# Performance work log

Hardware: AMD Instinct MI355X
Metric: run time of the kernel (lower is better)

Reference implementation:

```python
import jax, jax.numpy as jnp
import numpy as np

DIM, NH, T_MAX = 1024, 16, 2048
HD = DIM // NH
EPS = 1e-6


def _rope_tables(T, hd, dtype=jnp.float32):
    inv_freq = 1.0 / (10000.0 ** (jnp.arange(0, hd, 2, dtype=jnp.float32) / hd))
    t = jnp.arange(T, dtype=jnp.float32)
    freqs = jnp.outer(t, inv_freq)                 # [T, hd/2]
    emb = jnp.concatenate([freqs, freqs], axis=-1)  # [T, hd]
    return jnp.cos(emb).astype(dtype), jnp.sin(emb).astype(dtype)


def _rotate_half(x):
    x1, x2 = jnp.split(x, 2, axis=-1)
    return jnp.concatenate([-x2, x1], axis=-1)


def _rmsnorm(x, g):
    rms = jnp.sqrt(jnp.mean(x * x, axis=-1, keepdims=True) + EPS)
    return x / rms * g


def setup_inputs() -> dict:
    key = jax.random.key(0)
    ks = jax.random.split(key, 10)
    B, T, C = 4, 2048, DIM
    s = 1.0 / np.sqrt(C)
    x = jax.random.normal(ks[0], (B, T, C), dtype=jnp.float32)
    mask = jnp.tril(jnp.ones((T, T), dtype=jnp.int32))[None, None, :, :]
    wq = jax.random.normal(ks[1], (C, C), jnp.float32) * s
    wk = jax.random.normal(ks[2], (C, C), jnp.float32) * s
    wv = jax.random.normal(ks[3], (C, C), jnp.float32) * s
    wo = jax.random.normal(ks[4], (C, C), jnp.float32) * s
    w1 = jax.random.normal(ks[5], (C, 4 * C), jnp.float32) * s
    w2 = jax.random.normal(ks[6], (4 * C, C), jnp.float32) * (1.0 / np.sqrt(4 * C))
    w3 = jax.random.normal(ks[7], (C, 4 * C), jnp.float32) * s
    g1 = jnp.ones((C,), jnp.float32)
    g2 = jnp.ones((C,), jnp.float32)
    return {"x": x, "mask": mask, "g1": g1, "wq": wq, "wk": wk, "wv": wv,
            "wo": wo, "g2": g2, "w1": w1, "w2": w2, "w3": w3}


def reference(x, mask, g1, wq, wk, wv, wo, g2, w1, w2, w3):
    B, T, C = x.shape
    scale = HD ** -0.5
    # --- attention sublayer ---
    h = _rmsnorm(x, g1)
    q = (h @ wq).reshape(B, T, NH, HD)
    k = (h @ wk).reshape(B, T, NH, HD)
    v = (h @ wv).reshape(B, T, NH, HD)
    cos, sin = _rope_tables(T, HD, x.dtype)
    cos = cos[None, :, None, :]
    sin = sin[None, :, None, :]
    q = q * cos + _rotate_half(q) * sin
    k = k * cos + _rotate_half(k) * sin
    attn = jnp.einsum("bthd,bshd->bhts", q, k) * scale  # [B,H,T,T]
    attn = jnp.where(mask == 0, -jnp.inf, attn)
    attn = jax.nn.softmax(attn, axis=-1)
    o = jnp.einsum("bhts,bshd->bthd", attn, v).reshape(B, T, C)
    x = x + o @ wo
    # --- SwiGLU FFN sublayer ---
    h = _rmsnorm(x, g2)
    x = x + (jax.nn.silu(h @ w1) * (h @ w3)) @ w2
    return x
```

## Files before the change

kernel.cpp:

```cpp
#include <hip/hip_runtime.h>
#include <cstdint>

typedef unsigned short u16;
typedef __attribute__((ext_vector_type(8))) short bf16x8;
typedef __attribute__((ext_vector_type(4))) float f32x4;

__device__ __forceinline__ u16 f2b(float f) {
  union { float f; unsigned u; } c; c.f = f;
  unsigned u = c.u;
  return (u16)((u + 0x7FFFu + ((u >> 16) & 1u)) >> 16);
}
__device__ __forceinline__ float b2f(u16 b) {
  union { unsigned u; float f; } c; c.u = ((unsigned)b) << 16;
  return c.f;
}

typedef __attribute__((address_space(1))) void gv_t;
typedef __attribute__((address_space(3))) void lv_t;
__device__ __forceinline__ void gload_lds16(const void* g, void* l) {
  __builtin_amdgcn_global_load_lds((gv_t*)g, (lv_t*)l, 16, 0, 0);
}

__global__ void transpose_f2b(const float* __restrict__ in, u16* __restrict__ out,
                              int R, int C) {
  __shared__ float t[32][33];
  const int c0 = blockIdx.x * 32, r0 = blockIdx.y * 32;
  const int tx = threadIdx.x, ty = threadIdx.y;
#pragma unroll
  for (int i = 0; i < 4; ++i)
    t[ty + 8 * i][tx] = in[(size_t)(r0 + ty + 8 * i) * C + c0 + tx];
  __syncthreads();
#pragma unroll
  for (int i = 0; i < 4; ++i)
    out[(size_t)(c0 + ty + 8 * i) * R + r0 + tx] = f2b(t[tx][ty + 8 * i]);
}

__global__ __launch_bounds__(256) void rmsnorm_k(const float* __restrict__ x,
                                                 const float* __restrict__ g,
                                                 u16* __restrict__ out) {
  const int row = blockIdx.x, tid = threadIdx.x;
  const float4 v = ((const float4*)x)[(size_t)row * 256 + tid];
  float ss = v.x * v.x + v.y * v.y + v.z * v.z + v.w * v.w;
#pragma unroll
  for (int off = 1; off < 64; off <<= 1) ss += __shfl_xor(ss, off, 64);
  __shared__ float red[4];
  if ((tid & 63) == 0) red[tid >> 6] = ss;
  __syncthreads();
  const float mean = (red[0] + red[1] + red[2] + red[3]) * (1.0f / 1024.0f);
  const float rinv = 1.0f / sqrtf(mean + 1e-6f);
  const float4 gv = ((const float4*)g)[tid];
  u16* o = out + (size_t)row * 1024 + tid * 4;
  o[0] = f2b(v.x * rinv * gv.x);
  o[1] = f2b(v.y * rinv * gv.y);
  o[2] = f2b(v.z * rinv * gv.z);
  o[3] = f2b(v.w * rinv * gv.w);
}

__global__ __launch_bounds__(256) void rope_k(u16* __restrict__ qkv) {
  const int i = blockIdx.x * 256 + threadIdx.x;
  const int d = i & 31;
  const int h = (i >> 5) & 15;
  const int bt = i >> 9;
  const int t = bt & 2047;
  const float inv = exp2f((float)d * -0.4152410118609203f);
  const float th = (float)t * inv;
  float s, c;
  sincosf(th, &s, &c);
  size_t base = (size_t)bt * 3072 + h * 64 + d;
#pragma unroll
  for (int half = 0; half < 2; ++half) {
    const float x1 = b2f(qkv[base]);
    const float x2 = b2f(qkv[base + 32]);
    qkv[base]      = f2b(x1 * c - x2 * s);
    qkv[base + 32] = f2b(x2 * c + x1 * s);
    base += 1024;
  }
}

__global__ void vtrans_k(const u16* __restrict__ qkv, u16* __restrict__ VT) {
  __shared__ u16 tl[32][34];
  const int t0 = blockIdx.x * 32;
  const int bh = blockIdx.y >> 1;
  const int d0 = (blockIdx.y & 1) * 32;
  const int b = bh >> 4, h = bh & 15;
  const int tx = threadIdx.x, ty = threadIdx.y;
  const u16* src = qkv + (size_t)(b * 2048 + t0) * 3072 + 2048 + h * 64 + d0;
#pragma unroll
  for (int i = 0; i < 4; ++i)
    tl[ty + 8 * i][tx] = src[(size_t)(ty + 8 * i) * 3072 + tx];
  __syncthreads();
  u16* dst = VT + ((size_t)bh * 64 + d0) * 2048 + t0;
#pragma unroll
  for (int i = 0; i < 4; ++i)
    dst[(size_t)(ty + 8 * i) * 2048 + tx] = tl[tx][ty + 8 * i];
}

template <int EPI>
__global__ __launch_bounds__(256)
void gemm_bt(const u16* __restrict__ A, const u16* __restrict__ BT,
             void* __restrict__ Cout, const float* __restrict__ resid,
             int M, int N, int K, int lda) {
  __shared__ alignas(16) u16 As[128 * 32];
  __shared__ alignas(16) u16 Bs[128 * 32];
  const int tid = threadIdx.x;
  const int wave = tid >> 6, lane = tid & 63;
  const int wr = wave >> 1, wc = wave & 1;
  const int l15 = lane & 15, quad = lane >> 4;
  const int bm = blockIdx.x * 128, bn = blockIdx.y * 128;

  f32x4 acc[4][4];
#pragma unroll
  for (int i = 0; i < 4; ++i)
#pragma unroll
    for (int j = 0; j < 4; ++j) acc[i][j] = (f32x4){0.f, 0.f, 0.f, 0.f};

  const int srow = wave * 32 + (lane >> 2);
  const int scol = (lane & 3) * 8;
  const u16* gA0 = A + (size_t)(bm + srow) * lda + scol;
  const u16* gA1 = gA0 + (size_t)16 * lda;
  const u16* gB0 = BT + (size_t)(bn + srow) * K + scol;
  const u16* gB1 = gB0 + (size_t)16 * K;
  u16* lA0 = As + wave * 1024; u16* lA1 = lA0 + 512;
  u16* lB0 = Bs + wave * 1024; u16* lB1 = lB0 + 512;

  const u16* pa = As + (wr * 64 + l15) * 32 + quad * 8;
  const u16* pb = Bs + (wc * 64 + l15) * 32 + quad * 8;

  for (int kt = 0; kt < K; kt += 32) {
    gload_lds16(gA0 + kt, lA0);
    gload_lds16(gA1 + kt, lA1);
    gload_lds16(gB0 + kt, lB0);
    gload_lds16(gB1 + kt, lB1);
    __syncthreads();
    bf16x8 af[4], bfv[4];
#pragma unroll
    for (int i = 0; i < 4; ++i) af[i] = *(const bf16x8*)(pa + i * 512);
#pragma unroll
    for (int j = 0; j < 4; ++j) bfv[j] = *(const bf16x8*)(pb + j * 512);
#pragma unroll
    for (int i = 0; i < 4; ++i)
#pragma unroll
      for (int j = 0; j < 4; ++j)
        acc[i][j] = __builtin_amdgcn_mfma_f32_16x16x32_bf16(af[i], bfv[j], acc[i][j], 0, 0, 0);
    __syncthreads();
  }

#pragma unroll
  for (int i = 0; i < 4; ++i) {
    const int gr = bm + wr * 64 + i * 16 + quad * 4;
#pragma unroll
    for (int j = 0; j < 4; ++j) {
      const int gc = bn + wc * 64 + j * 16 + l15;
#pragma unroll
      for (int r = 0; r < 4; ++r) {
        const size_t off = (size_t)(gr + r) * N + gc;
        if (EPI == 0) {
          ((u16*)Cout)[off] = f2b(acc[i][j][r]);
        } else {
          ((float*)Cout)[off] = resid[off] + acc[i][j][r];
        }
      }
    }
  }
}

__global__ __launch_bounds__(256)
void attn_kernel(const u16* __restrict__ QKV, const u16* __restrict__ VT,
                 u16* __restrict__ O) {
  const int T = 2048, stQ = 3072;
  const int tid = threadIdx.x, wave = tid >> 6, lane = tid & 63;
  const int l15 = lane & 15, quad = lane >> 4;
  const int qt = (int)gridDim.x - 1 - (int)blockIdx.x;
  const int qb0 = qt * 128;
  const int bh = blockIdx.y, b = bh >> 4, h = bh & 15;
  const float sc2 = 0.125f * 1.44269504088896f;
  const float M0 = 32.0f;

  __shared__ alignas(16) u16 Kf[8 * 512];
  __shared__ alignas(16) u16 Vf[8 * 512];
  __shared__ alignas(16) u16 Pl[4][2][16 * 72];

  const u16* Qb  = QKV + (size_t)b * T * stQ + h * 64;
  const u16* Kb  = Qb + 1024;
  const u16* VTb = VT + (size_t)bh * 64 * T;

  const int r0 = qb0 + wave * 16;
  const int r1 = r0 + 64;
  const u16* qp0 = Qb + (size_t)(r0 + l15) * stQ + quad * 8;
  const u16* qp1 = Qb + (size_t)(r1 + l15) * stQ + quad * 8;
  const bf16x8 qf00 = *(const bf16x8*)qp0;
  const bf16x8 qf01 = *(const bf16x8*)(qp0 + 32);
  const bf16x8 qf10 = *(const bf16x8*)qp1;
  const bf16x8 qf11 = *(const bf16x8*)(qp1 + 32);

  bf16x8 ones;
#pragma unroll
  for (int j = 0; j < 8; ++j) ones[j] = (short)0x3F80;

  const u16* kS = Kb + (size_t)(wave * 16 + l15) * stQ + quad * 8;
  const u16* vS = VTb + (size_t)(wave * 16 + l15) * T + quad * 8;
  u16* kD0 = Kf + (wave * 2 + 0) * 512;  u16* kD1 = Kf + (wave * 2 + 1) * 512;
  u16* vD0 = Vf + (wave * 2 + 0) * 512;  u16* vD1 = Vf + (wave * 2 + 1) * 512;

  f32x4 o0[4], o1[4], sum0, sum1;
#pragma unroll
  for (int c = 0; c < 4; ++c) {
    o0[c] = (f32x4){0.f, 0.f, 0.f, 0.f};
    o1[c] = (f32x4){0.f, 0.f, 0.f, 0.f};
  }
  sum0 = (f32x4){0.f, 0.f, 0.f, 0.f};
  sum1 = (f32x4){0.f, 0.f, 0.f, 0.f};

  u16* pw0 = &Pl[wave][0][0];
  u16* pw1 = &Pl[wave][1][0];

  const int nkt = qt * 2 + 2;
  for (int kt = 0; kt < nkt; ++kt) {
    const int kb0 = kt * 64;
    gload_lds16(kS + (size_t)kb0 * stQ,      kD0);
    gload_lds16(kS + (size_t)kb0 * stQ + 32, kD1);
    gload_lds16(vS + kb0,                    vD0);
    gload_lds16(vS + kb0 + 32,               vD1);
    __syncthreads();

    bf16x8 kf[8];
#pragma unroll
    for (int g = 0; g < 8; ++g)
      kf[g] = *(const bf16x8*)(Kf + g * 512 + lane * 8);

    const bool act0 = (kb0 <= r0 + 15);

    {
      f32x4 s[4];
#pragma unroll
      for (int jj = 0; jj < 4; ++jj) {
        s[jj] = (f32x4){0.f, 0.f, 0.f, 0.f};
        s[jj] = __builtin_amdgcn_mfma_f32_16x16x32_bf16(qf10, kf[jj * 2 + 0], s[jj], 0, 0, 0);
        s[jj] = __builtin_amdgcn_mfma_f32_16x16x32_bf16(qf11, kf[jj * 2 + 1], s[jj], 0, 0, 0);
      }
      if (kb0 + 63 > r1) {
#pragma unroll
        for (int jj = 0; jj < 4; ++jj)
#pragma unroll
          for (int r = 0; r < 4; ++r) {
            const bool msk = (kb0 + jj * 16 + l15) > (r1 + quad * 4 + r);
            const float a = msk ? -1e30f : (s[jj][r] * sc2 - M0);
            pw1[(quad * 4 + r) * 72 + jj * 16 + l15] = f2b(exp2f(a));
          }
      } else {
#pragma unroll
        for (int jj = 0; jj < 4; ++jj)
#pragma unroll
          for (int r = 0; r < 4; ++r)
            pw1[(quad * 4 + r) * 72 + jj * 16 + l15] =
                f2b(exp2f(s[jj][r] * sc2 - M0));
      }
    }
    if (act0) {
      f32x4 s[4];
#pragma unroll
      for (int jj = 0; jj < 4; ++jj) {
        s[jj] = (f32x4){0.f, 0.f, 0.f, 0.f};
        s[jj] = __builtin_amdgcn_mfma_f32_16x16x32_bf16(qf00, kf[jj * 2 + 0], s[jj], 0, 0, 0);
        s[jj] = __builtin_amdgcn_mfma_f32_16x16x32_bf16(qf01, kf[jj * 2 + 1], s[jj], 0, 0, 0);
      }
      if (kb0 + 63 > r0) {
#pragma unroll
        for (int jj = 0; jj < 4; ++jj)
#pragma unroll
          for (int r = 0; r < 4; ++r) {
            const bool msk = (kb0 + jj * 16 + l15) > (r0 + quad * 4 + r);
            const float a = msk ? -1e30f : (s[jj][r] * sc2 - M0);
            pw0[(quad * 4 + r) * 72 + jj * 16 + l15] = f2b(exp2f(a));
          }
      } else {
#pragma unroll
        for (int jj = 0; jj < 4; ++jj)
#pragma unroll
          for (int r = 0; r < 4; ++r)
            pw0[(quad * 4 + r) * 72 + jj * 16 + l15] =
                f2b(exp2f(s[jj][r] * sc2 - M0));
      }
    }

    const bf16x8 pf10 = *(const bf16x8*)(pw1 + l15 * 72 + quad * 8);
    const bf16x8 pf11 = *(const bf16x8*)(pw1 + l15 * 72 + 32 + quad * 8);
#pragma unroll
    for (int c = 0; c < 4; ++c) {
      const bf16x8 v0 = *(const bf16x8*)(Vf + (c * 2 + 0) * 512 + lane * 8);
      const bf16x8 v1 = *(const bf16x8*)(Vf + (c * 2 + 1) * 512 + lane * 8);
      o1[c] = __builtin_amdgcn_mfma_f32_16x16x32_bf16(pf10, v0, o1[c], 0, 0, 0);
      o1[c] = __builtin_amdgcn_mfma_f32_16x16x32_bf16(pf11, v1, o1[c], 0, 0, 0);
    }
    sum1 = __builtin_amdgcn_mfma_f32_16x16x32_bf16(pf10, ones, sum1, 0, 0, 0);
    sum1 = __builtin_amdgcn_mfma_f32_16x16x32_bf16(pf11, ones, sum1, 0, 0, 0);
    if (act0) {
      const bf16x8 pf00 = *(const bf16x8*)(pw0 + l15 * 72 + quad * 8);
      const bf16x8 pf01 = *(const bf16x8*)(pw0 + l15 * 72 + 32 + quad * 8);
#pragma unroll
      for (int c = 0; c < 4; ++c) {
        const bf16x8 v0 = *(const bf16x8*)(Vf + (c * 2 + 0) * 512 + lane * 8);
        const bf16x8 v1 = *(const bf16x8*)(Vf + (c * 2 + 1) * 512 + lane * 8);
        o0[c] = __builtin_amdgcn_mfma_f32_16x16x32_bf16(pf00, v0, o0[c], 0, 0, 0);
        o0[c] = __builtin_amdgcn_mfma_f32_16x16x32_bf16(pf01, v1, o0[c], 0, 0, 0);
      }
      sum0 = __builtin_amdgcn_mfma_f32_16x16x32_bf16(pf00, ones, sum0, 0, 0, 0);
      sum0 = __builtin_amdgcn_mfma_f32_16x16x32_bf16(pf01, ones, sum0, 0, 0, 0);
    }
    __syncthreads();
  }

  float i0[4], i1[4];
#pragma unroll
  for (int r = 0; r < 4; ++r) { i0[r] = 1.f / sum0[r]; i1[r] = 1.f / sum1[r]; }
  u16* op0 = O + ((size_t)(b * T) + r0 + quad * 4) * 1024 + h * 64 + l15;
  u16* op1 = O + ((size_t)(b * T) + r1 + quad * 4) * 1024 + h * 64 + l15;
#pragma unroll
  for (int c = 0; c < 4; ++c)
#pragma unroll
    for (int r = 0; r < 4; ++r) {
      op0[(size_t)r * 1024 + c * 16] = f2b(o0[c][r] * i0[r]);
      op1[(size_t)r * 1024 + c * 16] = f2b(o1[c][r] * i1[r]);
    }
}

__global__ __launch_bounds__(256) void gate_k(u16* __restrict__ a13) {
  const size_t i = (size_t)blockIdx.x * 256 + threadIdx.x;
  const size_t row = i >> 9, c8 = (i & 511) * 8;
  u16* p1v = a13 + row * 8192 + c8;
  const u16* p3v = p1v + 4096;
  uint4 u1 = *(uint4*)p1v;
  const uint4 u3 = *(const uint4*)p3v;
  u16* p1 = (u16*)&u1;
  const u16* p3 = (const u16*)&u3;
#pragma unroll
  for (int j = 0; j < 8; ++j) {
    const float a = b2f(p1[j]);
    const float g = b2f(p3[j]);
    const float s = a / (1.f + __expf(-a));
    p1[j] = f2b(s * g);
  }
  *(uint4*)p1v = u1;
}

extern "C" void kernel_launch(void* const* d_in, const int* in_sizes, int n_in,
                              void* d_out, int out_size, void* d_ws, size_t ws_size,
                              hipStream_t stream) {
  const float* x  = (const float*)d_in[0];
  const float* g1 = (const float*)d_in[2];
  const float* wq = (const float*)d_in[3];
  const float* wk = (const float*)d_in[4];
  const float* wv = (const float*)d_in[5];
  const float* wo = (const float*)d_in[6];
  const float* g2 = (const float*)d_in[7];
  const float* w1 = (const float*)d_in[8];
  const float* w2 = (const float*)d_in[9];
  const float* w3 = (const float*)d_in[10];
  float* out = (float*)d_out;

  const int T = 2048, NH = 16, B = 4;
  const int M = B * T;
  const size_t MB = 1ull << 20;

  char* ws = (char*)d_ws;
  u16* hb    = (u16*)(ws);
  u16* wqkvT = (u16*)(ws + 16 * MB);
  u16* woT   = (u16*)(ws + 22 * MB);
  u16* w13T  = (u16*)(ws + 24 * MB);
  u16* w2T   = (u16*)(ws + 40 * MB);
  u16* qkv   = (u16*)(ws + 48 * MB);
  u16* VT    = (u16*)(ws + 96 * MB);
  u16* Ob    = (u16*)(ws + 112 * MB);
  u16* a13   = (u16*)(ws + 48 * MB);

  const dim3 tb(32, 8);
  transpose_f2b<<<dim3(32, 32),  tb, 0, stream>>>(wq, wqkvT,              1024, 1024);
  transpose_f2b<<<dim3(32, 32),  tb, 0, stream>>>(wk, wqkvT + 1024*1024,  1024, 1024);
  transpose_f2b<<<dim3(32, 32),  tb, 0, stream>>>(wv, wqkvT + 2048*1024,  1024, 1024);
  transpose_f2b<<<dim3(32, 32),  tb, 0, stream>>>(wo, woT, 1024, 1024);
  transpose_f2b<<<dim3(128, 32), tb, 0, stream>>>(w1, w13T,               1024, 4096);
  transpose_f2b<<<dim3(128, 32), tb, 0, stream>>>(w3, w13T + 4096*1024,   1024, 4096);
  transpose_f2b<<<dim3(32, 128), tb, 0, stream>>>(w2, w2T, 4096, 1024);

  rmsnorm_k<<<M, 256, 0, stream>>>(x, g1, hb);

  gemm_bt<0><<<dim3(64, 24), 256, 0, stream>>>(hb, wqkvT, qkv, nullptr, M, 3072, 1024, 1024);

  rope_k<<<16384, 256, 0, stream>>>(qkv);
  vtrans_k<<<dim3(64, 128), tb, 0, stream>>>(qkv, VT);

  attn_kernel<<<dim3(T / 128, B * NH), 256, 0, stream>>>(qkv, VT, Ob);

  gemm_bt<1><<<dim3(64, 8), 256, 0, stream>>>(Ob, woT, out, x, M, 1024, 1024, 1024);

  rmsnorm_k<<<M, 256, 0, stream>>>(out, g2, hb);

  gemm_bt<0><<<dim3(64, 64), 256, 0, stream>>>(hb, w13T, a13, nullptr, M, 8192, 1024, 1024);

  gate_k<<<16384, 256, 0, stream>>>(a13);

  gemm_bt<1><<<dim3(64, 8), 256, 0, stream>>>(a13, w2T, out, out, M, 1024, 4096, 8192);
}
```

Measured before the change: 769.7 us.

## Add 256x256-tile 8-wave GEMM with pipelined LDS staging for QKV and W13

Adds a new bf16 GEMM kernel that computes 256x256 output tiles with 512 threads. It double-buffers K-tiles in 128KB of LDS using direct global-to-LDS loads, uses a swizzled layout, and interleaves quarter-tile MFMA phases with prefetch under explicit barriers and waitcnts. The QKV and W1/W3 projections now use it instead of the 128x128 GEMM. The goal is more data reuse per tile and better overlap of memory traffic with MFMA work. In exchange there are fewer blocks, heavy register and LDS use per block, and many barriers.

```diff
diff --git a/kernel.cpp b/kernel.cpp
--- a/kernel.cpp
+++ b/kernel.cpp
@@ -158,6 +158,135 @@
           ((u16*)Cout)[off] = f2b(acc[i][j][r]);
         } else {
           ((float*)Cout)[off] = resid[off] + acc[i][j][r];
+        }
+      }
+    }
+  }
+}
+
+template <int EPI>
+__global__ __launch_bounds__(512, 2)
+void gemm256(const u16* __restrict__ A, const u16* __restrict__ BT,
+             void* __restrict__ Cout, const float* __restrict__ resid,
+             int M, int N, int K, int lda) {
+  __shared__ alignas(16) u16 LDS[65536];
+  char* const ldsc = (char*)LDS;
+  const int tid = threadIdx.x;
+  const int wave = tid >> 6, lane = tid & 63;
+  const int wr = wave >> 2, wc = wave & 3;
+  const int l15 = lane & 15, quad = lane >> 4;
+  const int bm = blockIdx.x * 256, bn = blockIdx.y * 256;
+  const int NT = K >> 6;
+  const int NIT = NT >> 1;
+
+  const int swz = (l15 & 8) << 2;
+  const int aoff = (((wr * 64 + l15) * 64 + quad * 16) ^ swz);
+  const int boff = (((wc * 32 + l15) * 64 + quad * 16) ^ swz) + 65536;
+
+  const int kperm = ((lane & 3) ^ ((lane >> 5) << 1)) * 8;
+  const u16* sA = A + (size_t)(bm + wave * 16 + (lane >> 2)) * lda + kperm;
+  const u16* sB = BT + (size_t)(bn + wave * 16 + (lane >> 2)) * K + kperm;
+  const size_t hA = (size_t)128 * lda;
+  const size_t hB = (size_t)128 * K;
+  const int dstW = wave * 1024;
+
+  f32x4 acc[8][4];
+#pragma unroll
+  for (int m = 0; m < 8; ++m)
+#pragma unroll
+    for (int n = 0; n < 4; ++n) acc[m][n] = (f32x4){0.f, 0.f, 0.f, 0.f};
+  bf16x8 a[4][2], b[2][2];
+
+#define STAGE(kt_, slot_, buf_)                                               \
+  if ((kt_) < NT) {                                                           \
+    const u16* s_ = (((slot_) & 1) ? sB + ((size_t)((slot_) >> 1)) * hB       \
+                                   : sA + ((size_t)((slot_) >> 1)) * hA) +    \
+                    (size_t)(kt_) * 64;                                       \
+    char* d_ = ldsc + (((slot_) & 1) ? 65536 : 0) + (buf_) * 32768 +          \
+               ((slot_) >> 1) * 16384 + dstW;                                 \
+    gload_lds16(s_, d_);                                                      \
+    gload_lds16(s_ + 32, d_ + 8192);                                          \
+  }
+
+#define LOAD_A(mh_, buf_)                                                     \
+  _Pragma("unroll") for (int mf = 0; mf < 4; ++mf)                            \
+      _Pragma("unroll") for (int kk = 0; kk < 2; ++kk)                        \
+          a[mf][kk] = *(const bf16x8*)(ldsc + aoff + (buf_) * 32768 +         \
+                                       (mh_) * 16384 + kk * 8192 + mf * 1024);
+
+#define LOAD_B(nh_, buf_)                                                     \
+  _Pragma("unroll") for (int nf = 0; nf < 2; ++nf)                            \
+      _Pragma("unroll") for (int kk = 0; kk < 2; ++kk)                        \
+          b[nf][kk] = *(const bf16x8*)(ldsc + boff + (buf_) * 32768 +         \
+                                       (nh_) * 16384 + kk * 8192 + nf * 1024);
+
+#define MMA(mh_, nh_)                                                         \
+  __builtin_amdgcn_s_setprio(1);                                              \
+  _Pragma("unroll") for (int mf = 0; mf < 4; ++mf)                            \
+      _Pragma("unroll") for (int nf = 0; nf < 2; ++nf)                        \
+          _Pragma("unroll") for (int kk = 0; kk < 2; ++kk)                    \
+              acc[(mh_) * 4 + mf][(nh_) * 2 + nf] =                           \
+                  __builtin_amdgcn_mfma_f32_16x16x32_bf16(                    \
+                      a[mf][kk], b[nf][kk],                                   \
+                      acc[(mh_) * 4 + mf][(nh_) * 2 + nf], 0, 0, 0);          \
+  __builtin_amdgcn_s_setprio(0);
+
+#define BAR() __builtin_amdgcn_s_barrier()
+#define DRAIN_LGKM()                                                          \
+  {                                                                           \
+    asm volatile("s_waitcnt lgkmcnt(0)" ::: "memory");                        \
+    __builtin_amdgcn_sched_barrier(0);                                        \
+  }
+
+  STAGE(0, 0, 0); STAGE(0, 1, 0); STAGE(0, 2, 0); STAGE(0, 3, 0);
+  STAGE(1, 0, 1); STAGE(1, 1, 1);
+  asm volatile("s_waitcnt vmcnt(4)" ::: "memory");
+  BAR();
+
+  for (int i = 0; i < NIT; ++i) {
+    const int t = 2 * i;
+    LOAD_A(0, 0); LOAD_B(0, 0); STAGE(t + 1, 2, 1);
+    BAR(); DRAIN_LGKM(); MMA(0, 0); BAR();
+    LOAD_B(1, 0); STAGE(t + 1, 3, 1);
+    BAR(); DRAIN_LGKM(); MMA(0, 1); BAR();
+    LOAD_A(1, 0); LOAD_B(0, 0); STAGE(t + 2, 0, 0);
+    BAR(); DRAIN_LGKM(); MMA(1, 0); BAR();
+    LOAD_B(1, 0); STAGE(t + 2, 1, 0);
+    BAR(); DRAIN_LGKM(); MMA(1, 1);
+    if (i == NIT - 1) { asm volatile("s_waitcnt vmcnt(0)" ::: "memory"); }
+    else              { asm volatile("s_waitcnt vmcnt(4)" ::: "memory"); }
+    BAR();
+    LOAD_A(0, 1); LOAD_B(0, 1); STAGE(t + 2, 2, 0);
+    BAR(); DRAIN_LGKM(); MMA(0, 0); BAR();
+    LOAD_B(1, 1); STAGE(t + 2, 3, 0);
+    BAR(); DRAIN_LGKM(); MMA(0, 1); BAR();
+    LOAD_A(1, 1); LOAD_B(0, 1); STAGE(t + 3, 0, 1);
+    BAR(); DRAIN_LGKM(); MMA(1, 0); BAR();
+    LOAD_B(1, 1); STAGE(t + 3, 1, 1);
+    BAR(); DRAIN_LGKM(); MMA(1, 1);
+    if (i < NIT - 1) { asm volatile("s_waitcnt vmcnt(4)" ::: "memory"); }
+    BAR();
+  }
+#undef STAGE
+#undef LOAD_A
+#undef LOAD_B
+#undef MMA
+#undef BAR
+#undef DRAIN_LGKM
+
+#pragma unroll
+  for (int m = 0; m < 8; ++m) {
+    const int gr = bm + (m >> 2) * 128 + wr * 64 + (m & 3) * 16 + quad * 4;
+#pragma unroll
+    for (int n = 0; n < 4; ++n) {
+      const int gc = bn + (n >> 1) * 128 + wc * 32 + (n & 1) * 16 + l15;
+#pragma unroll
+      for (int r = 0; r < 4; ++r) {
+        const size_t off = (size_t)(gr + r) * N + gc;
+        if (EPI == 0) {
+          ((u16*)Cout)[off] = f2b(acc[m][n][r]);
+        } else {
+          ((float*)Cout)[off] = resid[off] + acc[m][n][r];
         }
       }
     }
@@ -384,7 +513,7 @@
 
   rmsnorm_k<<<M, 256, 0, stream>>>(x, g1, hb);
 
-  gemm_bt<0><<<dim3(64, 24), 256, 0, stream>>>(hb, wqkvT, qkv, nullptr, M, 3072, 1024, 1024);
+  gemm256<0><<<dim3(32, 12), 512, 0, stream>>>(hb, wqkvT, qkv, nullptr, M, 3072, 1024, 1024);
 
   rope_k<<<16384, 256, 0, stream>>>(qkv);
   vtrans_k<<<dim3(64, 128), tb, 0, stream>>>(qkv, VT);
@@ -395,7 +524,7 @@
 
   rmsnorm_k<<<M, 256, 0, stream>>>(out, g2, hb);
 
-  gemm_bt<0><<<dim3(64, 64), 256, 0, stream>>>(hb, w13T, a13, nullptr, M, 8192, 1024, 1024);
+  gemm256<0><<<dim3(32, 32), 512, 0, stream>>>(hb, w13T, a13, nullptr, M, 8192, 1024, 1024);
 
   gate_k<<<16384, 256, 0, stream>>>(a13);
 
```

Result: faster. 722.7 us (-6.1%).
